# Optimization experiments

Measured on AMD Instinct MI355X. Metric: run time of the kernel, lower is better.

Reference implementation:

```python
import jax, jax.numpy as jnp
import numpy as np
import math

NUM_LEVEL = 16
LEVEL_DIM = 2
BASE_RES = 16
LOG2_T = 19
LEVEL_SCALE = 1.38191288
N_POINTS = 262144

_PRIMES = np.array([1, 2654435761, 805459861], dtype=np.uint32)  # tiny-cuda-nn hash primes
_CORNERS = np.array([[(c >> d) & 1 for d in range(3)] for c in range(8)], dtype=np.uint32)  # [8,3]


def _grid_meta():
    # mirrors GridEncoder.get_grid_info: per-level table offsets (aligned to 8)
    max_len = 2 ** LOG2_T
    offs = []
    off = 0
    for i in range(NUM_LEVEL):
        res = int(np.ceil(BASE_RES * LEVEL_SCALE ** i))
        p = min(max_len, res ** 3)
        p = int(np.ceil(p / 8) * 8)
        offs.append(off)
        off += p
    offs.append(off)
    return offs


def setup_inputs() -> dict:
    key = jax.random.key(0)
    k1, k2 = jax.random.split(key)
    offs = _grid_meta()
    # raw coords in [-1, 1); forward maps (x+1)/2 -> [0, 1)
    input_means = jax.random.uniform(k1, (N_POINTS, 3), dtype=jnp.float32) * 2.0 - 1.0
    # embeddings.data.uniform_(-0.01, 0.01)
    embeddings = jax.random.uniform(k2, (offs[-1], LEVEL_DIM), dtype=jnp.float32) * 0.02 - 0.01
    return {"input_means": input_means, "embeddings": embeddings}


def _encode(input_means, embeddings):
    x = (input_means + 1.0) / 2.0  # [N,3] in [0,1]
    offs = _grid_meta()
    lg_scale = math.log2(LEVEL_SCALE)
    corners = jnp.asarray(_CORNERS)  # [8,3]
    primes = jnp.asarray(_PRIMES)    # [3]
    outs = []
    for l in range(NUM_LEVEL):
        hsize = offs[l + 1] - offs[l]                    # table rows this level
        scale = 2.0 ** (l * lg_scale) * BASE_RES - 1.0   # align_corners=True
        res = int(math.ceil(scale)) + 1                  # grid resolution
        table = embeddings[offs[l]:offs[l + 1]]          # [hsize, C]
        pos = x * scale                                  # align_corners -> no +0.5
        pg = jnp.floor(pos)
        frac = pos - pg                                  # [N,3]
        pgu = pg.astype(jnp.uint32)
        cpos = pgu[:, None, :] + corners[None]           # [N,8,3] corner coords
        if res ** 3 > hsize:
            # hashed level: xor of coord*prime (uint32 wraparound)
            h = cpos * primes
            idx = h[..., 0] ^ h[..., 1] ^ h[..., 2]
        else:
            # dense (tiled) level
            r = jnp.uint32(res)
            idx = cpos[..., 0] + cpos[..., 1] * r + cpos[..., 2] * r * r
        idx = (idx % jnp.uint32(hsize)).astype(jnp.int32)
        feats = table[idx]                               # [N,8,C] gather
        w = jnp.where(corners[None] == 1, frac[:, None, :], 1.0 - frac[:, None, :]).prod(-1)  # [N,8]
        outs.append(jnp.einsum('nk,nkc->nc', w, feats))  # trilinear interp
    # matches ot_encod.permute(1,0,2).reshape(N, L*C): level-major feature concat
    return jnp.concatenate(outs, axis=-1)                # [N, L*C]


def reference(input_means, embeddings):
    return _encode(input_means, embeddings)
```

## Files before the change

### kernel.cpp

```cpp
#include <hip/hip_runtime.h>
#include <cmath>

#define NPTS 262144
#define NLVL 16
#define NDENSE 5
#define NHASH 11
#define HASH_MASK 0x7FFFFu

struct MetaD { float scale[NDENSE]; unsigned off[NDENSE]; unsigned res[NDENSE]; };
struct MetaH { float scale[NHASH]; unsigned off[NHASH]; };

__global__ __launch_bounds__(256) void enc_dense(
    const float* __restrict__ means, const float* __restrict__ emb,
    float2* __restrict__ dst, int lvl_major, MetaD meta)
{
    const int p = blockIdx.x * 256 + threadIdx.x;
    const int l = blockIdx.y;

    const float x = (means[3 * p + 0] + 1.0f) * 0.5f;
    const float y = (means[3 * p + 1] + 1.0f) * 0.5f;
    const float z = (means[3 * p + 2] + 1.0f) * 0.5f;

    const float s      = meta.scale[l];
    const unsigned off = meta.off[l];
    const unsigned r   = meta.res[l];

    const float px = x * s, py = y * s, pz = z * s;
    const float gx = floorf(px), gy = floorf(py), gz = floorf(pz);
    const float fx = px - gx, fy = py - gy, fz = pz - gz;
    const unsigned ix = (unsigned)gx, iy = (unsigned)gy, iz = (unsigned)gz;

    const unsigned base = ix + iy * r + iz * r * r + off;
    const unsigned dy = r, dz = r * r;

    const float2* __restrict__ emb2 = (const float2*)emb;
    float2 f[8];
    f[0] = emb2[base];           f[1] = emb2[base + 1];
    f[2] = emb2[base + dy];      f[3] = emb2[base + dy + 1];
    f[4] = emb2[base + dz];      f[5] = emb2[base + dz + 1];
    f[6] = emb2[base + dz + dy]; f[7] = emb2[base + dz + dy + 1];

    const float wx0 = 1.0f - fx, wy0 = 1.0f - fy, wz0 = 1.0f - fz;
    const float w00 = wz0 * wy0, w01 = wz0 * fy, w10 = fz * wy0, w11 = fz * fy;
    const float a0 = w00 * (wx0 * f[0].x + fx * f[1].x) + w01 * (wx0 * f[2].x + fx * f[3].x)
                   + w10 * (wx0 * f[4].x + fx * f[5].x) + w11 * (wx0 * f[6].x + fx * f[7].x);
    const float a1 = w00 * (wx0 * f[0].y + fx * f[1].y) + w01 * (wx0 * f[2].y + fx * f[3].y)
                   + w10 * (wx0 * f[4].y + fx * f[5].y) + w11 * (wx0 * f[6].y + fx * f[7].y);

    const size_t di = lvl_major ? ((size_t)l * NPTS + p) : ((size_t)p * NLVL + l);
    dst[di] = make_float2(a0, a1);
}

__device__ __forceinline__ float2 hash_level(
    const float* __restrict__ emb, unsigned off, float s,
    float x, float y, float z)
{
    const float px = x * s, py = y * s, pz = z * s;
    const float gx = floorf(px), gy = floorf(py), gz = floorf(pz);
    const float fx = px - gx, fy = py - gy, fz = pz - gz;
    const unsigned ix = (unsigned)gx, iy = (unsigned)gy, iz = (unsigned)gz;

    const unsigned hy0 = iy * 2654435761u, hy1 = hy0 + 2654435761u;
    const unsigned hz0 = iz * 805459861u,  hz1 = hz0 + 805459861u;
    const unsigned hyz[4] = {hy0 ^ hz0, hy1 ^ hz0, hy0 ^ hz1, hy1 ^ hz1};

    const float wy0 = 1.0f - fy, wz0 = 1.0f - fz;
    const float wc[4] = {wy0 * wz0, fy * wz0, wy0 * fz, fy * fz};
    const float wx0 = 1.0f - fx;

    const float2* __restrict__ emb2 = (const float2*)emb;
    const float4* __restrict__ emb4 = (const float4*)emb;

    float a0 = 0.0f, a1 = 0.0f;
    if ((ix & 1u) == 0u) {
#pragma unroll
        for (int c = 0; c < 4; ++c) {
            const unsigned i0 = (ix ^ hyz[c]) & HASH_MASK;
            const float4 f = emb4[(off + (i0 & ~1u)) >> 1];
            const bool sw = (i0 & 1u);
            const float c0x = sw ? f.z : f.x, c0y = sw ? f.w : f.y;
            const float c1x = sw ? f.x : f.z, c1y = sw ? f.y : f.w;
            a0 += wc[c] * (wx0 * c0x + fx * c1x);
            a1 += wc[c] * (wx0 * c0y + fx * c1y);
        }
    } else {
#pragma unroll
        for (int c = 0; c < 4; ++c) {
            const unsigned i0 = (ix        ^ hyz[c]) & HASH_MASK;
            const unsigned i1 = ((ix + 1u) ^ hyz[c]) & HASH_MASK;
            const float2 f0 = emb2[off + i0];
            const float2 f1 = emb2[off + i1];
            a0 += wc[c] * (wx0 * f0.x + fx * f1.x);
            a1 += wc[c] * (wx0 * f0.y + fx * f1.y);
        }
    }
    return make_float2(a0, a1);
}

__global__ __launch_bounds__(256) void enc_hash(
    const float* __restrict__ means, const float* __restrict__ emb,
    float2* __restrict__ dst, int lvl_major, MetaH meta)
{
    const unsigned b = blockIdx.x;
    const unsigned xcd = b & 7u, slot = b >> 3;
    unsigned il, chunk;
    if (slot < 512u) { il = xcd; chunk = slot; }
    else {
        if (xcd >= 6u) return;
        il = 8u + (xcd >> 1);
        chunk = ((slot - 512u) << 1) | (xcd & 1u);
    }
    const float s      = meta.scale[il];
    const unsigned off = meta.off[il];
    const unsigned lvl = il + NDENSE;

    const unsigned p0 = chunk * 512u + threadIdx.x;

#pragma unroll
    for (int pp = 0; pp < 2; ++pp) {
        const unsigned p = p0 + pp * 256u;
        const float x = (means[3 * p + 0] + 1.0f) * 0.5f;
        const float y = (means[3 * p + 1] + 1.0f) * 0.5f;
        const float z = (means[3 * p + 2] + 1.0f) * 0.5f;
        const float2 a = hash_level(emb, off, s, x, y, z);
        const size_t di = lvl_major ? ((size_t)lvl * NPTS + p) : ((size_t)p * NLVL + lvl);
        dst[di] = a;
    }
}

__global__ __launch_bounds__(256) void transpose_out(
    const float2* __restrict__ ws, float* __restrict__ out)
{
    const int p = blockIdx.x * 256 + threadIdx.x;
    float4 o[8];
    float2* o2 = (float2*)o;
#pragma unroll
    for (int l = 0; l < NLVL; ++l)
        o2[l] = ws[(size_t)l * NPTS + p];
    float4* out4 = (float4*)(out + (size_t)p * (2 * NLVL));
#pragma unroll
    for (int k = 0; k < 8; ++k)
        out4[k] = o[k];
}

extern "C" void kernel_launch(void* const* d_in, const int* in_sizes, int n_in,
                              void* d_out, int out_size, void* d_ws, size_t ws_size,
                              hipStream_t stream)
{
    const float* means = (const float*)d_in[0];
    const float* emb   = (const float*)d_in[1];
    float* out         = (float*)d_out;

    MetaD md;
    MetaH mh;
    const double lg = log2(1.38191288);
    unsigned off = 0;
    for (int l = 0; l < NLVL; ++l) {
        const double scale_d = pow(2.0, (double)l * lg) * 16.0 - 1.0;
        const unsigned res_enc = (unsigned)ceil(scale_d) + 1u;

        const double gres_d = ceil(16.0 * pow(1.38191288, (double)l));
        unsigned long long r3 = (unsigned long long)gres_d;
        r3 = r3 * r3 * r3;
        unsigned long long pl = r3 < (1ull << 19) ? r3 : (1ull << 19);
        pl = (pl + 7ull) / 8ull * 8ull;

        if (l < NDENSE) {
            md.scale[l] = (float)scale_d;
            md.off[l]   = off;
            md.res[l]   = res_enc;
        } else {
            mh.scale[l - NDENSE] = (float)scale_d;
            mh.off[l - NDENSE]   = off;
        }
        off += (unsigned)pl;
    }

    const size_t ws_needed = (size_t)NLVL * NPTS * sizeof(float2);
    const bool use_ws = ws_size >= ws_needed;
    float2* dst = use_ws ? (float2*)d_ws : (float2*)out;
    const int lvl_major = use_ws ? 1 : 0;

    enc_dense<<<dim3(NPTS / 256, NDENSE, 1), 256, 0, stream>>>(means, emb, dst, lvl_major, md);
    enc_hash <<<dim3(8 * 768, 1, 1),          256, 0, stream>>>(means, emb, dst, lvl_major, mh);
    if (use_ws)
        transpose_out<<<NPTS / 256, 256, 0, stream>>>((const float2*)d_ws, out);
}
```

Measured before the change: 204.0 us.

## Fuse dense levels into transpose pass and simplify hash-level gather scheduling

Dense-level encoding moves into the final transpose kernel, so the workspace holds only the 11 hash levels and the dense results never round-trip through memory. The hash kernel now does 4 points per thread with a contiguous level-chunk split across XCDs. It also drops the even-ix float4 pairing trick in favour of 8 independent float2 gathers. The aim is less workspace traffic and one fewer launch, at the cost of more work in the finalize kernel and possibly more gather transactions.

```diff
diff --git a/kernel.cpp b/kernel.cpp
--- a/kernel.cpp
+++ b/kernel.cpp
@@ -7,12 +7,131 @@
 #define NHASH 11
 #define HASH_MASK 0x7FFFFu
 
+#define PPT 4
+#define CHUNK (256 * PPT)
+#define CHUNKS_PER_LVL (NPTS / CHUNK)
+#define TOTAL_UNITS (NHASH * CHUNKS_PER_LVL)
+#define UNITS_PER_XCD (TOTAL_UNITS / 8)
+
 struct MetaD { float scale[NDENSE]; unsigned off[NDENSE]; unsigned res[NDENSE]; };
 struct MetaH { float scale[NHASH]; unsigned off[NHASH]; };
 
-__global__ __launch_bounds__(256) void enc_dense(
+__global__ __launch_bounds__(256) void enc_hash(
     const float* __restrict__ means, const float* __restrict__ emb,
-    float2* __restrict__ dst, int lvl_major, MetaD meta)
+    float2* __restrict__ dst, int lvl_major, MetaH meta)
+{
+    const unsigned b   = blockIdx.x;
+    const unsigned g   = (b & 7u) * UNITS_PER_XCD + (b >> 3);
+    const unsigned il  = g >> 8;
+    const unsigned chk = g & 255u;
+
+    const float sc     = meta.scale[il];
+    const unsigned off = meta.off[il];
+    const unsigned lvl = il + NDENSE;
+
+    const unsigned p0 = chk * CHUNK + threadIdx.x;
+    const float2* __restrict__ emb2 = (const float2*)emb;
+
+#pragma unroll
+    for (int pp = 0; pp < PPT; ++pp) {
+        const unsigned p = p0 + (unsigned)pp * 256u;
+
+        const float x = (means[3 * p + 0] + 1.0f) * 0.5f;
+        const float y = (means[3 * p + 1] + 1.0f) * 0.5f;
+        const float z = (means[3 * p + 2] + 1.0f) * 0.5f;
+
+        const float px = x * sc, py = y * sc, pz = z * sc;
+        const float gx = floorf(px), gy = floorf(py), gz = floorf(pz);
+        const float fx = px - gx, fy = py - gy, fz = pz - gz;
+        const unsigned ix = (unsigned)gx, iy = (unsigned)gy, iz = (unsigned)gz;
+
+        const unsigned hy0 = iy * 2654435761u, hy1 = hy0 + 2654435761u;
+        const unsigned hz0 = iz * 805459861u,  hz1 = hz0 + 805459861u;
+        const unsigned x0 = ix, x1 = ix + 1u;
+
+        unsigned idx[8];
+        idx[0] = (x0 ^ hy0 ^ hz0) & HASH_MASK;
+        idx[1] = (x1 ^ hy0 ^ hz0) & HASH_MASK;
+        idx[2] = (x0 ^ hy1 ^ hz0) & HASH_MASK;
+        idx[3] = (x1 ^ hy1 ^ hz0) & HASH_MASK;
+        idx[4] = (x0 ^ hy0 ^ hz1) & HASH_MASK;
+        idx[5] = (x1 ^ hy0 ^ hz1) & HASH_MASK;
+        idx[6] = (x0 ^ hy1 ^ hz1) & HASH_MASK;
+        idx[7] = (x1 ^ hy1 ^ hz1) & HASH_MASK;
+
+        float2 f[8];
+#pragma unroll
+        for (int c = 0; c < 8; ++c)
+            f[c] = emb2[off + idx[c]];
+
+        const float wx0 = 1.0f - fx, wy0 = 1.0f - fy, wz0 = 1.0f - fz;
+        const float w00 = wz0 * wy0, w01 = wz0 * fy, w10 = fz * wy0, w11 = fz * fy;
+        const float a0 = w00 * (wx0 * f[0].x + fx * f[1].x) + w01 * (wx0 * f[2].x + fx * f[3].x)
+                       + w10 * (wx0 * f[4].x + fx * f[5].x) + w11 * (wx0 * f[6].x + fx * f[7].x);
+        const float a1 = w00 * (wx0 * f[0].y + fx * f[1].y) + w01 * (wx0 * f[2].y + fx * f[3].y)
+                       + w10 * (wx0 * f[4].y + fx * f[5].y) + w11 * (wx0 * f[6].y + fx * f[7].y);
+
+        const size_t di = lvl_major ? ((size_t)il * NPTS + p) : ((size_t)p * NLVL + lvl);
+        dst[di] = make_float2(a0, a1);
+    }
+}
+
+__global__ __launch_bounds__(256) void finalize(
+    const float* __restrict__ means, const float* __restrict__ emb,
+    const float2* __restrict__ ws, float* __restrict__ out, MetaD meta)
+{
+    const int p = blockIdx.x * 256 + threadIdx.x;
+
+    float2 o2[NLVL];
+
+#pragma unroll
+    for (int il = 0; il < NHASH; ++il)
+        o2[NDENSE + il] = ws[(size_t)il * NPTS + p];
+
+    const float x = (means[3 * p + 0] + 1.0f) * 0.5f;
+    const float y = (means[3 * p + 1] + 1.0f) * 0.5f;
+    const float z = (means[3 * p + 2] + 1.0f) * 0.5f;
+
+    const float2* __restrict__ emb2 = (const float2*)emb;
+
+#pragma unroll
+    for (int l = 0; l < NDENSE; ++l) {
+        const float s      = meta.scale[l];
+        const unsigned off = meta.off[l];
+        const unsigned r   = meta.res[l];
+
+        const float px = x * s, py = y * s, pz = z * s;
+        const float gx = floorf(px), gy = floorf(py), gz = floorf(pz);
+        const float fx = px - gx, fy = py - gy, fz = pz - gz;
+        const unsigned ix = (unsigned)gx, iy = (unsigned)gy, iz = (unsigned)gz;
+
+        const unsigned base = ix + iy * r + iz * r * r + off;
+        const unsigned dy = r, dz = r * r;
+
+        float2 f[8];
+        f[0] = emb2[base];           f[1] = emb2[base + 1];
+        f[2] = emb2[base + dy];      f[3] = emb2[base + dy + 1];
+        f[4] = emb2[base + dz];      f[5] = emb2[base + dz + 1];
+        f[6] = emb2[base + dz + dy]; f[7] = emb2[base + dz + dy + 1];
+
+        const float wx0 = 1.0f - fx, wy0 = 1.0f - fy, wz0 = 1.0f - fz;
+        const float w00 = wz0 * wy0, w01 = wz0 * fy, w10 = fz * wy0, w11 = fz * fy;
+        o2[l].x = w00 * (wx0 * f[0].x + fx * f[1].x) + w01 * (wx0 * f[2].x + fx * f[3].x)
+                + w10 * (wx0 * f[4].x + fx * f[5].x) + w11 * (wx0 * f[6].x + fx * f[7].x);
+        o2[l].y = w00 * (wx0 * f[0].y + fx * f[1].y) + w01 * (wx0 * f[2].y + fx * f[3].y)
+                + w10 * (wx0 * f[4].y + fx * f[5].y) + w11 * (wx0 * f[6].y + fx * f[7].y);
+    }
+
+    float4* out4 = (float4*)(out + (size_t)p * (2 * NLVL));
+    const float4* src = (const float4*)o2;
+#pragma unroll
+    for (int k = 0; k < 8; ++k)
+        out4[k] = src[k];
+}
+
+__global__ __launch_bounds__(256) void enc_dense_direct(
+    const float* __restrict__ means, const float* __restrict__ emb,
+    float2* __restrict__ dst, MetaD meta)
 {
     const int p = blockIdx.x * 256 + threadIdx.x;
     const int l = blockIdx.y;
@@ -47,100 +166,7 @@
     const float a1 = w00 * (wx0 * f[0].y + fx * f[1].y) + w01 * (wx0 * f[2].y + fx * f[3].y)
                    + w10 * (wx0 * f[4].y + fx * f[5].y) + w11 * (wx0 * f[6].y + fx * f[7].y);
 
-    const size_t di = lvl_major ? ((size_t)l * NPTS + p) : ((size_t)p * NLVL + l);
-    dst[di] = make_float2(a0, a1);
-}
-
-__device__ __forceinline__ float2 hash_level(
-    const float* __restrict__ emb, unsigned off, float s,
-    float x, float y, float z)
-{
-    const float px = x * s, py = y * s, pz = z * s;
-    const float gx = floorf(px), gy = floorf(py), gz = floorf(pz);
-    const float fx = px - gx, fy = py - gy, fz = pz - gz;
-    const unsigned ix = (unsigned)gx, iy = (unsigned)gy, iz = (unsigned)gz;
-
-    const unsigned hy0 = iy * 2654435761u, hy1 = hy0 + 2654435761u;
-    const unsigned hz0 = iz * 805459861u,  hz1 = hz0 + 805459861u;
-    const unsigned hyz[4] = {hy0 ^ hz0, hy1 ^ hz0, hy0 ^ hz1, hy1 ^ hz1};
-
-    const float wy0 = 1.0f - fy, wz0 = 1.0f - fz;
-    const float wc[4] = {wy0 * wz0, fy * wz0, wy0 * fz, fy * fz};
-    const float wx0 = 1.0f - fx;
-
-    const float2* __restrict__ emb2 = (const float2*)emb;
-    const float4* __restrict__ emb4 = (const float4*)emb;
-
-    float a0 = 0.0f, a1 = 0.0f;
-    if ((ix & 1u) == 0u) {
-#pragma unroll
-        for (int c = 0; c < 4; ++c) {
-            const unsigned i0 = (ix ^ hyz[c]) & HASH_MASK;
-            const float4 f = emb4[(off + (i0 & ~1u)) >> 1];
-            const bool sw = (i0 & 1u);
-            const float c0x = sw ? f.z : f.x, c0y = sw ? f.w : f.y;
-            const float c1x = sw ? f.x : f.z, c1y = sw ? f.y : f.w;
-            a0 += wc[c] * (wx0 * c0x + fx * c1x);
-            a1 += wc[c] * (wx0 * c0y + fx * c1y);
-        }
-    } else {
-#pragma unroll
-        for (int c = 0; c < 4; ++c) {
-            const unsigned i0 = (ix        ^ hyz[c]) & HASH_MASK;
-            const unsigned i1 = ((ix + 1u) ^ hyz[c]) & HASH_MASK;
-            const float2 f0 = emb2[off + i0];
-            const float2 f1 = emb2[off + i1];
-            a0 += wc[c] * (wx0 * f0.x + fx * f1.x);
-            a1 += wc[c] * (wx0 * f0.y + fx * f1.y);
-        }
-    }
-    return make_float2(a0, a1);
-}
-
-__global__ __launch_bounds__(256) void enc_hash(
-    const float* __restrict__ means, const float* __restrict__ emb,
-    float2* __restrict__ dst, int lvl_major, MetaH meta)
-{
-    const unsigned b = blockIdx.x;
-    const unsigned xcd = b & 7u, slot = b >> 3;
-    unsigned il, chunk;
-    if (slot < 512u) { il = xcd; chunk = slot; }
-    else {
-        if (xcd >= 6u) return;
-        il = 8u + (xcd >> 1);
-        chunk = ((slot - 512u) << 1) | (xcd & 1u);
-    }
-    const float s      = meta.scale[il];
-    const unsigned off = meta.off[il];
-    const unsigned lvl = il + NDENSE;
-
-    const unsigned p0 = chunk * 512u + threadIdx.x;
-
-#pragma unroll
-    for (int pp = 0; pp < 2; ++pp) {
-        const unsigned p = p0 + pp * 256u;
-        const float x = (means[3 * p + 0] + 1.0f) * 0.5f;
-        const float y = (means[3 * p + 1] + 1.0f) * 0.5f;
-        const float z = (means[3 * p + 2] + 1.0f) * 0.5f;
-        const float2 a = hash_level(emb, off, s, x, y, z);
-        const size_t di = lvl_major ? ((size_t)lvl * NPTS + p) : ((size_t)p * NLVL + lvl);
-        dst[di] = a;
-    }
-}
-
-__global__ __launch_bounds__(256) void transpose_out(
-    const float2* __restrict__ ws, float* __restrict__ out)
-{
-    const int p = blockIdx.x * 256 + threadIdx.x;
-    float4 o[8];
-    float2* o2 = (float2*)o;
-#pragma unroll
-    for (int l = 0; l < NLVL; ++l)
-        o2[l] = ws[(size_t)l * NPTS + p];
-    float4* out4 = (float4*)(out + (size_t)p * (2 * NLVL));
-#pragma unroll
-    for (int k = 0; k < 8; ++k)
-        out4[k] = o[k];
+    dst[(size_t)p * NLVL + l] = make_float2(a0, a1);
 }
 
 extern "C" void kernel_launch(void* const* d_in, const int* in_sizes, int n_in,
@@ -176,13 +202,13 @@
         off += (unsigned)pl;
     }
 
-    const size_t ws_needed = (size_t)NLVL * NPTS * sizeof(float2);
-    const bool use_ws = ws_size >= ws_needed;
-    float2* dst = use_ws ? (float2*)d_ws : (float2*)out;
-    const int lvl_major = use_ws ? 1 : 0;
-
-    enc_dense<<<dim3(NPTS / 256, NDENSE, 1), 256, 0, stream>>>(means, emb, dst, lvl_major, md);
-    enc_hash <<<dim3(8 * 768, 1, 1),          256, 0, stream>>>(means, emb, dst, lvl_major, mh);
-    if (use_ws)
-        transpose_out<<<NPTS / 256, 256, 0, stream>>>((const float2*)d_ws, out);
-}
+    const size_t ws_needed = (size_t)NHASH * NPTS * sizeof(float2);
+    if (ws_size >= ws_needed) {
+        float2* ws = (float2*)d_ws;
+        enc_hash<<<TOTAL_UNITS, 256, 0, stream>>>(means, emb, ws, 1, mh);
+        finalize<<<NPTS / 256, 256, 0, stream>>>(means, emb, ws, out, md);
+    } else {
+        enc_hash<<<TOTAL_UNITS, 256, 0, stream>>>(means, emb, (float2*)out, 0, mh);
+        enc_dense_direct<<<dim3(NPTS / 256, NDENSE, 1), 256, 0, stream>>>(means, emb, (float2*)out, md);
+    }
+}
```

Result: slower. 212.0 us (+3.9%).
